# Optimization experiments

Measured on AMD Instinct MI355X. Metric: run time of the kernel, lower is better.

Reference implementation:

```python
import jax, jax.numpy as jnp
import numpy as np

K = 4            # branching factor of the complete dependency tree
LEVELS = 8       # depths 0..7
N = (K**LEVELS - 1) // (K - 1)   # 21845 nodes, levels stored contiguously
D = 128
NUM_POS = 18     # universal POS tags -> pos_params ModuleList size
NUM_DEP = 46     # dependency relations -> dep_params ModuleList size


def level_start(l):
    # index of first node at depth l (breadth-first layout)
    return (K**l - 1) // (K - 1)


def setup_inputs() -> dict:
    key = jax.random.key(0)
    ks = jax.random.split(key, 7)
    emb = jax.random.normal(ks[0], (N, D), jnp.float32)
    pos_ids = jax.random.randint(ks[1], (N,), 0, NUM_POS)
    dep_ids = jax.random.randint(ks[2], (N,), 0, NUM_DEP)  # dep tag of edge to parent
    s = 1.0 / np.sqrt(D)  # torch nn.Linear default init range
    pos_W = jax.random.uniform(ks[3], (NUM_POS, D, D), jnp.float32, -s, s)
    pos_b = jax.random.uniform(ks[4], (NUM_POS, D), jnp.float32, -s, s)
    dep_W = jax.random.uniform(ks[5], (NUM_DEP, D, D), jnp.float32, -s, s)
    dep_b = jax.random.uniform(ks[6], (NUM_DEP, D), jnp.float32, -s, s)
    return {"emb": emb, "pos_ids": pos_ids, "dep_ids": dep_ids,
            "pos_W": pos_W, "pos_b": pos_b, "dep_W": dep_W, "dep_b": dep_b}


def reference(emb, pos_ids, dep_ids, pos_W, pos_b, dep_W, dep_b) -> jnp.ndarray:
    # x_i = relu(PosLinear_{pos_i}(emb_i)) for every node (batched typed linear
    # via per-node weight gather: the memory-bound gather this module implies)
    x = jax.nn.relu(jnp.einsum('nd,nde->ne', emb, pos_W[pos_ids]) + pos_b[pos_ids])

    # bottom-up level sweep; leaves have no children so z = x there
    lo = level_start(LEVELS - 1)
    z = x[lo:lo + K**(LEVELS - 1)]            # [n_leaf, D]
    for l in range(LEVELS - 2, -1, -1):
        cs = level_start(l + 1)
        n_c = K**(l + 1)
        did = dep_ids[cs:cs + n_c]
        # z_c -> relu(DepLinear_{dep_c}(z_c)) for every child of this level
        u = jax.nn.relu(jnp.einsum('nd,nde->ne', z, dep_W[did]) + dep_b[did])
        # max over the K children of each parent, then max with parent's x
        u = u.reshape(K**l, K, D).max(axis=1)
        s = level_start(l)
        z = jnp.maximum(x[s:s + K**l], u)
    return z[0]  # root sentence embedding [D]
```

## Files before the change

### kernel.cpp

```cpp
#include <hip/hip_runtime.h>


#define DD 128
#define NN 21845
#define NPOS 18
#define NDEP 46
#define NB 248
#define NCHALL 21844
#define CH_LO 20
#define NITEMS (NN + NCHALL - CH_LO)

typedef __attribute__((ext_vector_type(8))) short short8;
typedef __attribute__((ext_vector_type(4))) float f32x4;

__device__ __forceinline__ unsigned short f2bf(float f) {
    union { float f; unsigned int u; } v; v.f = f;
    unsigned int r = v.u + 0x7fffu + ((v.u >> 16) & 1u);
    return (unsigned short)(r >> 16);
}
__device__ __forceinline__ float bf2f(unsigned short s) {
    union { unsigned int u; float f; } v; v.u = ((unsigned int)s) << 16;
    return v.f;
}

__global__ __launch_bounds__(1024) void prep_kernel(
        const float* __restrict__ posW, const float* __restrict__ depW,
        unsigned short* __restrict__ Wt,
        const int* __restrict__ pos_ids, const int* __restrict__ dep_ids,
        int* __restrict__ perm_pos, int* __restrict__ perm_dep,
        int* __restrict__ ntiles, int2* __restrict__ tbl1,
        int2* __restrict__ tblL) {
    __shared__ __align__(16) char smem[9216];
    int bid = blockIdx.x, tid = threadIdx.x;
    if (bid >= 1) {
        unsigned short (*lds)[72] = (unsigned short (*)[72])smem;
        int mb = bid - 1;
        int mat = mb >> 2, tile = mb & 3;
        int tk = (tile >> 1) * 64, tn = (tile & 1) * 64;
        const float* W = (mat < NPOS) ? (posW + (size_t)mat * DD * DD)
                                      : (depW + (size_t)(mat - NPOS) * DD * DD);
        unsigned short* O = Wt + (size_t)mat * DD * DD;
        int tx = tid & 63, ty = tid >> 6;
#pragma unroll
        for (int i = 0; i < 4; ++i) {
            int r = i * 16 + ty;
            lds[tx][r] = f2bf(W[(size_t)(tk + r) * DD + tn + tx]);
        }
        __syncthreads();
#pragma unroll
        for (int i = 0; i < 4; ++i) {
            int r = i * 16 + ty;
            O[(size_t)(tn + r) * DD + tk + tx] = lds[r][tx];
        }
        return;
    }
    int* cnt  = (int*)smem;
    int* scb  = cnt + NB;
    int* tpre = scb + NB;
    int* rank = tpre + NB;
    for (int i = tid; i < NB; i += 1024) { cnt[i] = 0; rank[i] = 0; }
    __syncthreads();
    for (int g = tid; g < NITEMS; g += 1024) {
        int b;
        if (g < NN) {
            b = pos_ids[g];
        } else {
            int j = g - NN + CH_LO;
            int base = CH_LO, sz = 64, l = 2;
            while (j >= base + sz) { base += sz; sz <<= 2; ++l; }
            int c = j - base;
            b = NPOS + (l - 2) * NDEP + dep_ids[base + 1 + c];
        }
        atomicAdd(&cnt[b], 1);
    }
    __syncthreads();
    if (tid == 0) {
        const int gb[6] = {0, 20, 84, 340, 1364, 5460};
        int b = 0;
        for (int g = 0; g < 6; ++g) {
            int w = (g == 0) ? NPOS : NDEP;
            int off = gb[g], tp = 0;
            for (int i = 0; i < w; ++i, ++b) {
                scb[b] = off; tpre[b] = tp;
                off += cnt[b]; tp += (cnt[b] + 63) >> 6;
            }
            ntiles[g] = tp;
        }
    }
    __syncthreads();
    if (tid < NB) {
        int b = tid;
        int g = (b < NPOS) ? 0 : 1 + (b - NPOS) / NDEP;
        int loc = (b < NPOS) ? b : (b - NPOS) % NDEP;
        int2* tb = (g == 0) ? tbl1 : tblL + (g - 1) * 302;
        int c = cnt[b];
        int t = (c + 63) >> 6;
        for (int k = 0; k < t; ++k) {
            int2 ent;
            ent.x = loc | (min(64, c - (k << 6)) << 8);
            ent.y = scb[b] + (k << 6);
            tb[tpre[b] + k] = ent;
        }
    }
    __syncthreads();
    for (int g = tid; g < NITEMS; g += 1024) {
        int b, payload;
        if (g < NN) {
            b = pos_ids[g]; payload = g;
        } else {
            int j = g - NN + CH_LO;
            int base = CH_LO, sz = 64, l = 2;
            while (j >= base + sz) { base += sz; sz <<= 2; ++l; }
            int c = j - base;
            b = NPOS + (l - 2) * NDEP + dep_ids[base + 1 + c];
            payload = c;
        }
        int r = atomicAdd(&rank[b], 1);
        int idx = scb[b] + r;
        if (b < NPOS) perm_pos[idx] = payload;
        else perm_dep[idx] = payload;
    }
}

template <int MODE>
__global__ __launch_bounds__(256) void gemm_kernel(
        const int2* __restrict__ tbl, const int* __restrict__ ntp,
        const int* __restrict__ perm, const unsigned short* __restrict__ Wt,
        const float* __restrict__ bias, const float* __restrict__ embf,
        const unsigned short* __restrict__ xb, const unsigned short* __restrict__ uprev,
        unsigned short* __restrict__ outr) {
    int nt = ntp[0];
    if ((int)blockIdx.x >= nt) return;
    int2 e = tbl[blockIdx.x];
    int bucket = e.x & 255;
    int rows = e.x >> 8;
    int rowstart = e.y;
    int lane = threadIdx.x & 63;
    int w = threadIdx.x >> 6;
    int lr = lane & 15;
    int kk = (lane >> 4) * 8;
    const short8 zero8 = {0, 0, 0, 0, 0, 0, 0, 0};

    int m_a = w * 16 + lr;
    bool valid_a = m_a < rows;
    int rid_a = valid_a ? perm[rowstart + m_a] : 0;

    short8 afr[4];
    if (MODE == 0) {
        const float* ar = embf + (size_t)rid_a * DD + kk;
#pragma unroll
        for (int s = 0; s < 4; ++s) {
            float4 lo = *(const float4*)(ar + s * 32);
            float4 hi = *(const float4*)(ar + s * 32 + 4);
            short8 a;
            a[0] = (short)f2bf(lo.x); a[1] = (short)f2bf(lo.y);
            a[2] = (short)f2bf(lo.z); a[3] = (short)f2bf(lo.w);
            a[4] = (short)f2bf(hi.x); a[5] = (short)f2bf(hi.y);
            a[6] = (short)f2bf(hi.z); a[7] = (short)f2bf(hi.w);
            afr[s] = valid_a ? a : zero8;
        }
    } else if (MODE == 1) {
        const unsigned short* ar = xb + (size_t)rid_a * DD + kk;
#pragma unroll
        for (int s = 0; s < 4; ++s)
            afr[s] = valid_a ? *(const short8*)(ar + s * 32) : zero8;
    } else {
        const unsigned short* xr = xb + (size_t)rid_a * DD + kk;
        const unsigned short* ur = uprev + (size_t)(4 * rid_a) * DD + kk;
#pragma unroll
        for (int s = 0; s < 4; ++s) {
            short8 a = *(const short8*)(xr + s * 32);
#pragma unroll
            for (int j = 0; j < 4; ++j) {
                short8 u = *(const short8*)(ur + j * DD + s * 32);
#pragma unroll
                for (int q = 0; q < 8; ++q)
                    if ((unsigned short)u[q] > (unsigned short)a[q]) a[q] = u[q];
            }
            afr[s] = valid_a ? a : zero8;
        }
    }

    f32x4 acc[8];
#pragma unroll
    for (int t = 0; t < 8; ++t) acc[t] = (f32x4){0.f, 0.f, 0.f, 0.f};

    const unsigned short* Wb = Wt + (size_t)bucket * DD * DD;
#pragma unroll
    for (int s = 0; s < 4; ++s) {
        short8 bfr[8];
#pragma unroll
        for (int t = 0; t < 8; ++t)
            bfr[t] = *(const short8*)(Wb + (size_t)(t * 16 + lr) * DD + s * 32 + kk);
#pragma unroll
        for (int t = 0; t < 8; ++t)
            acc[t] = __builtin_amdgcn_mfma_f32_16x16x32_bf16(afr[s], bfr[t], acc[t], 0, 0, 0);
    }

    int rq[4]; bool vq[4];
#pragma unroll
    for (int q = 0; q < 4; ++q) {
        int m = w * 16 + (lane >> 4) * 4 + q;
        vq[q] = m < rows;
        rq[q] = vq[q] ? perm[rowstart + m] : 0;
    }
    const float* bb = bias + bucket * DD;
#pragma unroll
    for (int t = 0; t < 8; ++t) {
        int col = t * 16 + lr;
        float bv = bb[col];
#pragma unroll
        for (int q = 0; q < 4; ++q) {
            if (vq[q]) {
                float v = fmaxf(acc[t][q] + bv, 0.f);
                outr[(size_t)rq[q] * DD + col] = f2bf(v);
            }
        }
    }
}

__global__ __launch_bounds__(1024) void tail_kernel(
        const int* __restrict__ dep_ids, const float* __restrict__ depW,
        const float* __restrict__ dep_b, const unsigned short* __restrict__ xbf,
        unsigned short* __restrict__ uarena, float* __restrict__ out) {
    __shared__ float zbuf[8][DD];
    int team = threadIdx.x >> 7, e = threadIdx.x & 127;
    {
        const unsigned short* up = uarena + (size_t)21760 * DD;
        unsigned short* uc = uarena + (size_t)21824 * DD;
        for (int rnd = 0; rnd < 2; ++rnd) {
            int c = team + rnd * 8;
            unsigned short m = xbf[(size_t)(5 + c) * DD + e];
#pragma unroll
            for (int j = 0; j < 4; ++j) {
                unsigned short u = up[(size_t)(4 * c + j) * DD + e];
                if (u > m) m = u;
            }
            zbuf[team][e] = bf2f(m);
            __syncthreads();
            int did = dep_ids[5 + c];
            const float* W = depW + (size_t)did * DD * DD;
            float a = dep_b[did * DD + e];
#pragma unroll 8
            for (int k = 0; k < DD; ++k)
                a = fmaf(zbuf[team][k], W[(size_t)k * DD + e], a);
            uc[(size_t)c * DD + e] = f2bf(fmaxf(a, 0.f));
            __syncthreads();
        }
    }
    {
        const unsigned short* up = uarena + (size_t)21824 * DD;
        unsigned short* uc = uarena + (size_t)21840 * DD;
        int c = team;
        if (team < 4) {
            unsigned short m = xbf[(size_t)(1 + c) * DD + e];
#pragma unroll
            for (int j = 0; j < 4; ++j) {
                unsigned short u = up[(size_t)(4 * c + j) * DD + e];
                if (u > m) m = u;
            }
            zbuf[team][e] = bf2f(m);
        }
        __syncthreads();
        if (team < 4) {
            int did = dep_ids[1 + c];
            const float* W = depW + (size_t)did * DD * DD;
            float a = dep_b[did * DD + e];
#pragma unroll 8
            for (int k = 0; k < DD; ++k)
                a = fmaf(zbuf[team][k], W[(size_t)k * DD + e], a);
            uc[(size_t)c * DD + e] = f2bf(fmaxf(a, 0.f));
        }
        __syncthreads();
    }
    if (threadIdx.x < DD) {
        unsigned short m = xbf[threadIdx.x];
#pragma unroll
        for (int j = 0; j < 4; ++j) {
            unsigned short u = uarena[(size_t)(21840 + j) * DD + threadIdx.x];
            if (u > m) m = u;
        }
        out[threadIdx.x] = bf2f(m);
    }
}

extern "C" void kernel_launch(void* const* d_in, const int* in_sizes, int n_in,
                              void* d_out, int out_size, void* d_ws, size_t ws_size,
                              hipStream_t stream) {
    const float* emb     = (const float*)d_in[0];
    const int*   pos_ids = (const int*)d_in[1];
    const int*   dep_ids = (const int*)d_in[2];
    const float* pos_W   = (const float*)d_in[3];
    const float* pos_b   = (const float*)d_in[4];
    const float* dep_W   = (const float*)d_in[5];
    const float* dep_b   = (const float*)d_in[6];
    float* out = (float*)d_out;

    char* p = (char*)d_ws;
    auto alloc = [&](size_t bytes) {
        char* r = p; p += (bytes + 255) & ~(size_t)255; return r;
    };
    int*  ntiles   = (int*)alloc(8 * 4);
    int*  perm_pos = (int*)alloc((size_t)NN * 4);
    int*  perm_dep = (int*)alloc((size_t)NCHALL * 4);
    int2* tbl1     = (int2*)alloc(360 * 8);
    int2* tblL     = (int2*)alloc(5 * 302 * 8);
    unsigned short* Wt     = (unsigned short*)alloc((size_t)64 * DD * DD * 2);
    unsigned short* xbf    = (unsigned short*)alloc((size_t)NN * DD * 2);
    unsigned short* uarena = (unsigned short*)alloc((size_t)NCHALL * DD * 2);

    prep_kernel<<<257, 1024, 0, stream>>>(pos_W, dep_W, Wt, pos_ids, dep_ids,
                                          perm_pos, perm_dep, ntiles, tbl1, tblL);
    gemm_kernel<0><<<360, 256, 0, stream>>>(tbl1, ntiles + 0, perm_pos, Wt, pos_b,
                                            emb, nullptr, nullptr, xbf);
    const unsigned short* Wtd = Wt + (size_t)NPOS * DD * DD;
    gemm_kernel<1><<<302, 256, 0, stream>>>(tblL + 4 * 302, ntiles + 5, perm_dep,
                                            Wtd, dep_b, nullptr,
                                            xbf + (size_t)5461 * DD, nullptr,
                                            uarena);
    gemm_kernel<2><<<110, 256, 0, stream>>>(tblL + 3 * 302, ntiles + 4, perm_dep,
                                            Wtd, dep_b, nullptr,
                                            xbf + (size_t)1365 * DD, uarena,
                                            uarena + (size_t)16384 * DD);
    gemm_kernel<2><<<62, 256, 0, stream>>>(tblL + 2 * 302, ntiles + 3, perm_dep,
                                           Wtd, dep_b, nullptr,
                                           xbf + (size_t)341 * DD,
                                           uarena + (size_t)16384 * DD,
                                           uarena + (size_t)20480 * DD);
    gemm_kernel<2><<<50, 256, 0, stream>>>(tblL + 1 * 302, ntiles + 2, perm_dep,
                                           Wtd, dep_b, nullptr,
                                           xbf + (size_t)85 * DD,
                                           uarena + (size_t)20480 * DD,
                                           uarena + (size_t)21504 * DD);
    gemm_kernel<2><<<46, 256, 0, stream>>>(tblL + 0 * 302, ntiles + 1, perm_dep,
                                           Wtd, dep_b, nullptr,
                                           xbf + (size_t)21 * DD,
                                           uarena + (size_t)21504 * DD,
                                           uarena + (size_t)21760 * DD);
    tail_kernel<<<1, 1024, 0, stream>>>(dep_ids, dep_W, dep_b, xbf, uarena, out);
}
```

Measured before the change: 209.7 us.

## Parallelize bucketing across blocks and fold small tree levels into tail kernel

The single-block histogram and scatter in the prep kernel are replaced by a multi-block histogram, fused with the weight conversion, followed by a multi-block plan and scatter kernel that uses per-block prefix counts. The two smallest dep-level GEMM launches move into the single-block tail kernel, which runs them with four 256-thread teams and removes two launches. The tail also reads the bf16 transposed weights with vector loads instead of fp32 strided reads. The risk is that the small levels now run on one CU rather than being spread across many blocks, and that the plan kernel sums the per-block counts redundantly in every block.

```diff
diff --git a/kernel.cpp b/kernel.cpp
--- a/kernel.cpp
+++ b/kernel.cpp
@@ -9,6 +9,7 @@
 #define NCHALL 21844
 #define CH_LO 20
 #define NITEMS (NN + NCHALL - CH_LO)
+#define NHB 171
 
 typedef __attribute__((ext_vector_type(8))) short short8;
 typedef __attribute__((ext_vector_type(4))) float f32x4;
@@ -23,78 +24,109 @@
     return v.f;
 }
 
-__global__ __launch_bounds__(1024) void prep_kernel(
+__device__ __forceinline__ void decode_item(int g, const int* __restrict__ pos_ids,
+                                            const int* __restrict__ dep_ids,
+                                            int& b, int& payload) {
+    if (g < NN) {
+        b = pos_ids[g]; payload = g;
+    } else {
+        int j = g - NN + CH_LO;
+        int base = CH_LO, sz = 64, l = 2;
+        while (j >= base + sz) { base += sz; sz <<= 2; ++l; }
+        int c = j - base;
+        b = NPOS + (l - 2) * NDEP + dep_ids[base + 1 + c];
+        payload = c;
+    }
+}
+
+__global__ __launch_bounds__(256) void conv_hist_kernel(
         const float* __restrict__ posW, const float* __restrict__ depW,
         unsigned short* __restrict__ Wt,
         const int* __restrict__ pos_ids, const int* __restrict__ dep_ids,
-        int* __restrict__ perm_pos, int* __restrict__ perm_dep,
-        int* __restrict__ ntiles, int2* __restrict__ tbl1,
-        int2* __restrict__ tblL) {
+        int* __restrict__ blk_cnt) {
     __shared__ __align__(16) char smem[9216];
     int bid = blockIdx.x, tid = threadIdx.x;
-    if (bid >= 1) {
+    if (bid < 256) {
         unsigned short (*lds)[72] = (unsigned short (*)[72])smem;
-        int mb = bid - 1;
-        int mat = mb >> 2, tile = mb & 3;
+        int mat = bid >> 2, tile = bid & 3;
         int tk = (tile >> 1) * 64, tn = (tile & 1) * 64;
         const float* W = (mat < NPOS) ? (posW + (size_t)mat * DD * DD)
                                       : (depW + (size_t)(mat - NPOS) * DD * DD);
         unsigned short* O = Wt + (size_t)mat * DD * DD;
         int tx = tid & 63, ty = tid >> 6;
 #pragma unroll
-        for (int i = 0; i < 4; ++i) {
-            int r = i * 16 + ty;
+        for (int i = 0; i < 16; ++i) {
+            int r = ty + i * 4;
             lds[tx][r] = f2bf(W[(size_t)(tk + r) * DD + tn + tx]);
         }
         __syncthreads();
 #pragma unroll
-        for (int i = 0; i < 4; ++i) {
-            int r = i * 16 + ty;
+        for (int i = 0; i < 16; ++i) {
+            int r = ty + i * 4;
             O[(size_t)(tn + r) * DD + tk + tx] = lds[r][tx];
         }
-        return;
-    }
-    int* cnt  = (int*)smem;
-    int* scb  = cnt + NB;
-    int* tpre = scb + NB;
-    int* rank = tpre + NB;
-    for (int i = tid; i < NB; i += 1024) { cnt[i] = 0; rank[i] = 0; }
-    __syncthreads();
-    for (int g = tid; g < NITEMS; g += 1024) {
-        int b;
-        if (g < NN) {
-            b = pos_ids[g];
-        } else {
-            int j = g - NN + CH_LO;
-            int base = CH_LO, sz = 64, l = 2;
-            while (j >= base + sz) { base += sz; sz <<= 2; ++l; }
-            int c = j - base;
-            b = NPOS + (l - 2) * NDEP + dep_ids[base + 1 + c];
-        }
-        atomicAdd(&cnt[b], 1);
-    }
-    __syncthreads();
-    if (tid == 0) {
-        const int gb[6] = {0, 20, 84, 340, 1364, 5460};
-        int b = 0;
-        for (int g = 0; g < 6; ++g) {
-            int w = (g == 0) ? NPOS : NDEP;
-            int off = gb[g], tp = 0;
-            for (int i = 0; i < w; ++i, ++b) {
-                scb[b] = off; tpre[b] = tp;
-                off += cnt[b]; tp += (cnt[b] + 63) >> 6;
-            }
-            ntiles[g] = tp;
-        }
+    } else {
+        int* h = (int*)smem;
+        for (int i = tid; i < NB; i += 256) h[i] = 0;
+        __syncthreads();
+        int hb = bid - 256;
+        int g = hb * 256 + tid;
+        if (g < NITEMS) {
+            int b, payload;
+            decode_item(g, pos_ids, dep_ids, b, payload);
+            atomicAdd(&h[b], 1);
+        }
+        __syncthreads();
+        for (int i = tid; i < NB; i += 256)
+            blk_cnt[hb * NB + i] = h[i];
+    }
+}
+
+__global__ __launch_bounds__(256) void plan_scatter_kernel(
+        const int* __restrict__ pos_ids, const int* __restrict__ dep_ids,
+        const int* __restrict__ blk_cnt, int* __restrict__ perm_pos,
+        int* __restrict__ perm_dep, int* __restrict__ ntiles,
+        int2* __restrict__ tbl1, int2* __restrict__ tblL) {
+    __shared__ int tot[NB], pre[NB], scb[NB], tpre[NB], rank[NB];
+    int bid = blockIdx.x, tid = threadIdx.x;
+    if (tid < NB) {
+        int sa = 0, sb = 0;
+        for (int bb = 0; bb < NHB; ++bb) {
+            int v = blk_cnt[bb * NB + tid];
+            sa += v;
+            if (bb < bid) sb += v;
+        }
+        tot[tid] = sa; pre[tid] = sb; rank[tid] = 0;
     }
     __syncthreads();
     if (tid < NB) {
+        const int gbase[5] = {20, 84, 340, 1364, 5460};
+        int gs, base;
+        if (tid < NPOS) { gs = 0; base = 0; }
+        else {
+            int g = (tid - NPOS) / NDEP;
+            gs = NPOS + g * NDEP; base = gbase[g];
+        }
+        int off = base, tp = 0;
+        for (int j = gs; j < tid; ++j) {
+            off += tot[j];
+            tp += (tot[j] + 63) >> 6;
+        }
+        scb[tid] = off; tpre[tid] = tp;
+        bool last = (tid == NPOS - 1) ||
+                    (tid >= NPOS && ((tid - NPOS) % NDEP == NDEP - 1));
+        if (bid == 0 && last) {
+            int g = (tid < NPOS) ? 0 : 1 + (tid - NPOS) / NDEP;
+            ntiles[g] = tp + ((tot[tid] + 63) >> 6);
+        }
+    }
+    __syncthreads();
+    if (bid == 0 && tid < NB) {
         int b = tid;
         int g = (b < NPOS) ? 0 : 1 + (b - NPOS) / NDEP;
         int loc = (b < NPOS) ? b : (b - NPOS) % NDEP;
         int2* tb = (g == 0) ? tbl1 : tblL + (g - 1) * 302;
-        int c = cnt[b];
-        int t = (c + 63) >> 6;
+        int c = tot[b], t = (c + 63) >> 6;
         for (int k = 0; k < t; ++k) {
             int2 ent;
             ent.x = loc | (min(64, c - (k << 6)) << 8);
@@ -102,41 +134,28 @@
             tb[tpre[b] + k] = ent;
         }
     }
-    __syncthreads();
-    for (int g = tid; g < NITEMS; g += 1024) {
+    int g = bid * 256 + tid;
+    if (g < NITEMS) {
         int b, payload;
-        if (g < NN) {
-            b = pos_ids[g]; payload = g;
-        } else {
-            int j = g - NN + CH_LO;
-            int base = CH_LO, sz = 64, l = 2;
-            while (j >= base + sz) { base += sz; sz <<= 2; ++l; }
-            int c = j - base;
-            b = NPOS + (l - 2) * NDEP + dep_ids[base + 1 + c];
-            payload = c;
-        }
-        int r = atomicAdd(&rank[b], 1);
-        int idx = scb[b] + r;
+        decode_item(g, pos_ids, dep_ids, b, payload);
+        int local = atomicAdd(&rank[b], 1);
+        int idx = scb[b] + pre[b] + local;
         if (b < NPOS) perm_pos[idx] = payload;
         else perm_dep[idx] = payload;
     }
 }
 
 template <int MODE>
-__global__ __launch_bounds__(256) void gemm_kernel(
-        const int2* __restrict__ tbl, const int* __restrict__ ntp,
-        const int* __restrict__ perm, const unsigned short* __restrict__ Wt,
+__device__ __forceinline__ void gemm_tile(
+        int2 e, const int* __restrict__ perm, const unsigned short* __restrict__ Wt,
         const float* __restrict__ bias, const float* __restrict__ embf,
         const unsigned short* __restrict__ xb, const unsigned short* __restrict__ uprev,
-        unsigned short* __restrict__ outr) {
-    int nt = ntp[0];
-    if ((int)blockIdx.x >= nt) return;
-    int2 e = tbl[blockIdx.x];
+        unsigned short* __restrict__ outr, int ltid) {
     int bucket = e.x & 255;
     int rows = e.x >> 8;
     int rowstart = e.y;
-    int lane = threadIdx.x & 63;
-    int w = threadIdx.x >> 6;
+    int lane = ltid & 63;
+    int w = ltid >> 6;
     int lr = lane & 15;
     int kk = (lane >> 4) * 8;
     const short8 zero8 = {0, 0, 0, 0, 0, 0, 0, 0};
@@ -219,68 +238,110 @@
     }
 }
 
+template <int MODE>
+__global__ __launch_bounds__(256) void gemm_kernel(
+        const int2* __restrict__ tbl, const int* __restrict__ ntp,
+        const int* __restrict__ perm, const unsigned short* __restrict__ Wt,
+        const float* __restrict__ bias, const float* __restrict__ embf,
+        const unsigned short* __restrict__ xb, const unsigned short* __restrict__ uprev,
+        unsigned short* __restrict__ outr) {
+    if ((int)blockIdx.x >= ntp[0]) return;
+    gemm_tile<MODE>(tbl[blockIdx.x], perm, Wt, bias, embf, xb, uprev, outr,
+                    threadIdx.x);
+}
+
 __global__ __launch_bounds__(1024) void tail_kernel(
-        const int* __restrict__ dep_ids, const float* __restrict__ depW,
-        const float* __restrict__ dep_b, const unsigned short* __restrict__ xbf,
-        unsigned short* __restrict__ uarena, float* __restrict__ out) {
-    __shared__ float zbuf[8][DD];
-    int team = threadIdx.x >> 7, e = threadIdx.x & 127;
+        const int2* __restrict__ tblL, const int* __restrict__ ntiles,
+        const int* __restrict__ perm_dep, const int* __restrict__ dep_ids,
+        const unsigned short* __restrict__ Wtd, const float* __restrict__ dep_b,
+        const unsigned short* __restrict__ xbf, unsigned short* __restrict__ uarena,
+        float* __restrict__ out) {
+    __shared__ float zbuf[16][DD];
+    int tid = threadIdx.x;
+    int team = tid >> 8, ltid = tid & 255;
+    unsigned short* uL4 = uarena + (size_t)20480 * DD;
+    unsigned short* uL3 = uarena + (size_t)21504 * DD;
+    unsigned short* uL2 = uarena + (size_t)21760 * DD;
+    unsigned short* uL1 = uarena + (size_t)21824 * DD;
+    unsigned short* uL0 = uarena + (size_t)21840 * DD;
+
+    int nt3 = ntiles[2];
+    for (int t = team; t < nt3; t += 4)
+        gemm_tile<2>(tblL[1 * 302 + t], perm_dep, Wtd, dep_b, nullptr,
+                     xbf + (size_t)85 * DD, uL4, uL3, ltid);
+    __syncthreads();
+    int nt2 = ntiles[1];
+    for (int t = team; t < nt2; t += 4)
+        gemm_tile<2>(tblL[0 * 302 + t], perm_dep, Wtd, dep_b, nullptr,
+                     xbf + (size_t)21 * DD, uL3, uL2, ltid);
+    __syncthreads();
+
     {
-        const unsigned short* up = uarena + (size_t)21760 * DD;
-        unsigned short* uc = uarena + (size_t)21824 * DD;
-        for (int rnd = 0; rnd < 2; ++rnd) {
-            int c = team + rnd * 8;
-            unsigned short m = xbf[(size_t)(5 + c) * DD + e];
+        int c = tid >> 7, e = tid & 127;
+#pragma unroll
+        for (int r = 0; r < 2; ++r) {
+            int cc = c + r * 8;
+            unsigned short m = xbf[(size_t)(5 + cc) * DD + e];
 #pragma unroll
             for (int j = 0; j < 4; ++j) {
-                unsigned short u = up[(size_t)(4 * c + j) * DD + e];
+                unsigned short u = uL2[(size_t)(4 * cc + j) * DD + e];
                 if (u > m) m = u;
             }
-            zbuf[team][e] = bf2f(m);
-            __syncthreads();
-            int did = dep_ids[5 + c];
-            const float* W = depW + (size_t)did * DD * DD;
+            zbuf[cc][e] = bf2f(m);
+        }
+        __syncthreads();
+#pragma unroll
+        for (int r = 0; r < 2; ++r) {
+            int cc = c + r * 8;
+            int did = dep_ids[5 + cc];
+            const unsigned short* Wr = Wtd + (size_t)did * DD * DD + (size_t)e * DD;
             float a = dep_b[did * DD + e];
-#pragma unroll 8
-            for (int k = 0; k < DD; ++k)
-                a = fmaf(zbuf[team][k], W[(size_t)k * DD + e], a);
-            uc[(size_t)c * DD + e] = f2bf(fmaxf(a, 0.f));
-            __syncthreads();
-        }
+#pragma unroll
+            for (int s = 0; s < 16; ++s) {
+                short8 w8 = *(const short8*)(Wr + s * 8);
+#pragma unroll
+                for (int q = 0; q < 8; ++q)
+                    a = fmaf(zbuf[cc][s * 8 + q], bf2f((unsigned short)w8[q]), a);
+            }
+            uL1[(size_t)cc * DD + e] = f2bf(fmaxf(a, 0.f));
+        }
+        __syncthreads();
     }
     {
-        const unsigned short* up = uarena + (size_t)21824 * DD;
-        unsigned short* uc = uarena + (size_t)21840 * DD;
-        int c = team;
-        if (team < 4) {
+        int c = tid >> 7, e = tid & 127;
+        if (c < 4) {
             unsigned short m = xbf[(size_t)(1 + c) * DD + e];
 #pragma unroll
             for (int j = 0; j < 4; ++j) {
-                unsigned short u = up[(size_t)(4 * c + j) * DD + e];
+                unsigned short u = uL1[(size_t)(4 * c + j) * DD + e];
                 if (u > m) m = u;
             }
-            zbuf[team][e] = bf2f(m);
-        }
-        __syncthreads();
-        if (team < 4) {
+            zbuf[c][e] = bf2f(m);
+        }
+        __syncthreads();
+        if (c < 4) {
             int did = dep_ids[1 + c];
-            const float* W = depW + (size_t)did * DD * DD;
+            const unsigned short* Wr = Wtd + (size_t)did * DD * DD + (size_t)e * DD;
             float a = dep_b[did * DD + e];
-#pragma unroll 8
-            for (int k = 0; k < DD; ++k)
-                a = fmaf(zbuf[team][k], W[(size_t)k * DD + e], a);
-            uc[(size_t)c * DD + e] = f2bf(fmaxf(a, 0.f));
-        }
-        __syncthreads();
-    }
-    if (threadIdx.x < DD) {
-        unsigned short m = xbf[threadIdx.x];
+#pragma unroll
+            for (int s = 0; s < 16; ++s) {
+                short8 w8 = *(const short8*)(Wr + s * 8);
+#pragma unroll
+                for (int q = 0; q < 8; ++q)
+                    a = fmaf(zbuf[c][s * 8 + q], bf2f((unsigned short)w8[q]), a);
+            }
+            uL0[(size_t)c * DD + e] = f2bf(fmaxf(a, 0.f));
+        }
+        __syncthreads();
+    }
+    if (tid < DD) {
+        unsigned short m = xbf[tid];
 #pragma unroll
         for (int j = 0; j < 4; ++j) {
-            unsigned short u = uarena[(size_t)(21840 + j) * DD + threadIdx.x];
+            unsigned short u = uL0[(size_t)j * DD + tid];
             if (u > m) m = u;
         }
-        out[threadIdx.x] = bf2f(m);
+        out[tid] = bf2f(m);
     }
 }
 
@@ -300,6 +361,7 @@
     auto alloc = [&](size_t bytes) {
         char* r = p; p += (bytes + 255) & ~(size_t)255; return r;
     };
+    int*  blk_cnt  = (int*)alloc((size_t)NHB * NB * 4);
     int*  ntiles   = (int*)alloc(8 * 4);
     int*  perm_pos = (int*)alloc((size_t)NN * 4);
     int*  perm_dep = (int*)alloc((size_t)NCHALL * 4);
@@ -309,8 +371,11 @@
     unsigned short* xbf    = (unsigned short*)alloc((size_t)NN * DD * 2);
     unsigned short* uarena = (unsigned short*)alloc((size_t)NCHALL * DD * 2);
 
-    prep_kernel<<<257, 1024, 0, stream>>>(pos_W, dep_W, Wt, pos_ids, dep_ids,
-                                          perm_pos, perm_dep, ntiles, tbl1, tblL);
+    conv_hist_kernel<<<256 + NHB, 256, 0, stream>>>(pos_W, dep_W, Wt, pos_ids,
+                                                    dep_ids, blk_cnt);
+    plan_scatter_kernel<<<NHB, 256, 0, stream>>>(pos_ids, dep_ids, blk_cnt,
+                                                 perm_pos, perm_dep, ntiles,
+                                                 tbl1, tblL);
     gemm_kernel<0><<<360, 256, 0, stream>>>(tbl1, ntiles + 0, perm_pos, Wt, pos_b,
                                             emb, nullptr, nullptr, xbf);
     const unsigned short* Wtd = Wt + (size_t)NPOS * DD * DD;
@@ -327,15 +392,6 @@
                                            xbf + (size_t)341 * DD,
                                            uarena + (size_t)16384 * DD,
                                            uarena + (size_t)20480 * DD);
-    gemm_kernel<2><<<50, 256, 0, stream>>>(tblL + 1 * 302, ntiles + 2, perm_dep,
-                                           Wtd, dep_b, nullptr,
-                                           xbf + (size_t)85 * DD,
-                                           uarena + (size_t)20480 * DD,
-                                           uarena + (size_t)21504 * DD);
-    gemm_kernel<2><<<46, 256, 0, stream>>>(tblL + 0 * 302, ntiles + 1, perm_dep,
-                                           Wtd, dep_b, nullptr,
-                                           xbf + (size_t)21 * DD,
-                                           uarena + (size_t)21504 * DD,
-                                           uarena + (size_t)21760 * DD);
-    tail_kernel<<<1, 1024, 0, stream>>>(dep_ids, dep_W, dep_b, xbf, uarena, out);
-}
+    tail_kernel<<<1, 1024, 0, stream>>>(tblL, ntiles, perm_dep, dep_ids, Wtd,
+                                        dep_b, xbf, uarena, out);
+}
```

After: 613.5 us. 2.93x slower.
